# Kernel tuning notes

Hardware: AMD Instinct MI355X
Metric: run time of the kernel (lower is better)

The kernel has to match this reference:

```python
import jax, jax.numpy as jnp
import numpy as np

NUM_LAYERS = 4
HID = 512
BATCH = 32
SEQ = 2048


def log_g(x):
    # log of the g() activation used by minGRU: g(x) = x+0.5 for x>=0, sigmoid(x) for x<0
    return jnp.where(x >= 0, jnp.log(jax.nn.relu(x) + 0.5), -jax.nn.softplus(-x))


def parallel_scan_log(log_coeffs, log_values):
    # log_coeffs: (B, T, H), log_values: (B, T+1, H); returns h: (B, T, H)
    a_star = jnp.cumsum(jnp.pad(log_coeffs, ((0, 0), (1, 0), (0, 0))), axis=1)  # (B, T+1, H)
    log_h = a_star + jax.lax.cumlogsumexp(log_values - a_star, axis=1)
    return jnp.exp(log_h)[:, 1:]


def setup_inputs() -> dict:
    key = jax.random.key(0)
    ks = jax.random.split(key, 4)
    x = jax.random.normal(ks[0], (BATCH, SEQ, HID), dtype=jnp.float32)
    h0 = jax.random.uniform(ks[1], (NUM_LAYERS, BATCH, HID), dtype=jnp.float32)
    scale = 0.02
    Wz = jax.random.normal(ks[2], (NUM_LAYERS, HID, HID), dtype=jnp.float32) * scale
    Wh = jax.random.normal(ks[3], (NUM_LAYERS, HID, HID), dtype=jnp.float32) * scale
    bz = jnp.zeros((NUM_LAYERS, HID), dtype=jnp.float32)
    bh = jnp.zeros((NUM_LAYERS, HID), dtype=jnp.float32)
    gamma = jnp.ones((NUM_LAYERS, HID), dtype=jnp.float32)
    beta = jnp.zeros((NUM_LAYERS, HID), dtype=jnp.float32)
    return {"x": x, "h0": h0, "Wz": Wz, "bz": bz, "Wh": Wh, "bh": bh, "gamma": gamma, "beta": beta}


def layernorm(x, g, b, eps=1e-5):
    mu = jnp.mean(x, axis=-1, keepdims=True)
    var = jnp.mean((x - mu) ** 2, axis=-1, keepdims=True)
    return (x - mu) * jax.lax.rsqrt(var + eps) * g + b


def reference(x, h0, Wz, bz, Wh, bh, gamma, beta):
    cur = x
    hiddens = []
    L = Wz.shape[0]
    for i in range(L):
        k = jnp.einsum('btd,dh->bth', cur, Wz[i]) + bz[i]
        log_z = -jax.nn.softplus(-k)          # log(sigmoid(k)) = log(z)
        log_coeffs = -jax.nn.softplus(k)      # log(1-z)
        log_tilde_h = log_g(jnp.einsum('btd,dh->bth', cur, Wh[i]) + bh[i])
        log_h0 = log_g(h0[i])[:, None, :]     # (B, 1, H)
        log_values = jnp.concatenate([log_h0, log_z + log_tilde_h], axis=1)
        h = parallel_scan_log(log_coeffs, log_values)  # (B, T, H)
        hiddens.append(h[:, -1])
        out = layernorm(h, gamma[i], beta[i])
        cur = out + cur  # res_proj is Identity since input_size == hidden_size
    return cur, jnp.stack(hiddens, axis=0)
```

## Files before the change

kernel.cpp:

```cpp
#include <hip/hip_runtime.h>
#include <stdint.h>

typedef unsigned short u16;
typedef __bf16 bf16x8 __attribute__((ext_vector_type(8)));
typedef float f32x4 __attribute__((ext_vector_type(4)));

#define HID 512
#define BATCH 32
#define SEQ 2048
#define NLAYERS 4
#define BT (BATCH*SEQ)
#define CHUNKS 64
#define TC (SEQ/CHUNKS)

__device__ __forceinline__ float bf2f(uint32_t lo) {
  union { uint32_t u; float f; } c; c.u = lo << 16; return c.f;
}
__device__ __forceinline__ uint32_t f2bf(float f) {
  union { float f; uint32_t u; } c; c.f = f;
  return (c.u + 0x7fffu + ((c.u >> 16) & 1u)) >> 16;
}
__device__ __forceinline__ uint32_t pk_bf16(float lo, float hi) {
  uint32_t r;
  asm("v_cvt_pk_bf16_f32 %0, %1, %2" : "=v"(r) : "v"(lo), "v"(hi));
  return r;
}
__device__ __forceinline__ float fast_rcp(float x) { return __builtin_amdgcn_rcpf(x); }

__device__ __forceinline__ void gload_lds16(const u16* g, u16* l) {
  __builtin_amdgcn_global_load_lds((__attribute__((address_space(1))) void*)g,
                                   (__attribute__((address_space(3))) void*)l, 16, 0, 0);
}

__global__ __launch_bounds__(256) void conv_weights(const float* __restrict__ Wz,
                                                    const float* __restrict__ Wh,
                                                    u16* __restrict__ Wt) {
  __shared__ float tile[64][65];
  const int l = blockIdx.z;
  const int k0 = blockIdx.x * 64;
  const int n0 = blockIdx.y * 64;
  const float* W = (n0 < 512 ? Wz : Wh) + (size_t)l * HID * HID;
  const int nc0 = (n0 < 512) ? n0 : n0 - 512;
  const int tx = threadIdx.x & 63, ty = threadIdx.x >> 6;
  for (int r = ty; r < 64; r += 4) tile[r][tx] = W[(size_t)(k0 + r) * HID + nc0 + tx];
  __syncthreads();
  for (int r = ty; r < 64; r += 4)
    Wt[((size_t)l * 1024 + n0 + r) * HID + k0 + tx] = (u16)f2bf(tile[tx][r]);
}

__global__ __launch_bounds__(256) void conv_x(const float* __restrict__ x, u16* __restrict__ xb) {
  size_t i = ((size_t)blockIdx.x * 256 + threadIdx.x) * 4;
  float4 f = *(const float4*)(x + i);
  uint2 o;
  o.x = pk_bf16(f.x, f.y);
  o.y = pk_bf16(f.z, f.w);
  *(uint2*)(xb + i) = o;
}

__global__ __launch_bounds__(512) void gemm_av(const u16* __restrict__ Ab,
                                               const u16* __restrict__ Btw,
                                               const float* __restrict__ bz,
                                               const float* __restrict__ bhp,
                                               uint32_t* __restrict__ av,
                                               float* __restrict__ Ac,
                                               float* __restrict__ Bc) {
  __shared__ __align__(16) u16 As[2][2][8192];
  __shared__ __align__(16) u16 Bs[2][2][8192];

  const int bid = blockIdx.x;
  const int xcd = bid & 7, rr_ = bid >> 3;
  const int mt = (rr_ >> 2) * 8 + xcd;
  const int nt = rr_ & 3;
  const int m0 = mt * 256;

  const int tid = threadIdx.x;
  const int lane = tid & 63, wv = tid >> 6;
  const int wm = wv >> 2, wn = wv & 3;
  const int l15 = lane & 15, quad = lane >> 4;
  const int rx = l15 & 7;
  const int bhalf = wn >> 1;

  const int aro0 = l15 * 64 + ((quad ^ rx) * 8);
  const int aro1 = l15 * 64 + (((4 + quad) ^ rx) * 8);
  const int bro0 = ((wn & 1) * 64 + l15) * 64 + ((quad ^ rx) * 8);
  const int bro1 = ((wn & 1) * 64 + l15) * 64 + (((4 + quad) ^ rx) * 8);

  const int srow = tid >> 3;
  const int kslot = (lane & 7) ^ (srow & 7);
  const u16* aS = Ab + (size_t)(m0 + srow) * HID + kslot * 8;
  const int qb = (srow >> 5) & 1, jb = srow & 31;
  const u16* bS = Btw + (size_t)(qb * 512 + nt * 128 + jb) * HID + kslot * 8;

  f32x4 acc[8][4];
#pragma unroll
  for (int i = 0; i < 8; ++i)
#pragma unroll
    for (int j = 0; j < 4; ++j) acc[i][j] = (f32x4){0.f, 0.f, 0.f, 0.f};
  bf16x8 afr[4][2], bfr[4][2];

#define STG_A(T, H, D) if ((T) < 8) { \
    gload_lds16(aS + (size_t)((H)*65536 + (T)*64), &As[D][H][wv*512]); \
    gload_lds16(aS + (size_t)((H)*65536 + 32768 + (T)*64), &As[D][H][4096 + wv*512]); }
#define STG_B(T, H, D) if ((T) < 8) { \
    gload_lds16(bS + (size_t)((H)*32768 + (T)*64), &Bs[D][H][wv*512]); \
    gload_lds16(bS + (size_t)((H)*32768 + 16384 + (T)*64), &Bs[D][H][4096 + wv*512]); }
#define LDA4(D, MB) { \
    _Pragma("unroll") for (int m_ = 0; m_ < 4; ++m_) \
    _Pragma("unroll") for (int k_ = 0; k_ < 2; ++k_) \
      afr[m_][k_] = *(const bf16x8*)&As[D][wm][((MB)+m_)*1024 + (k_ ? aro1 : aro0)]; }
#define LDB2(D, NB) { \
    _Pragma("unroll") for (int n_ = 0; n_ < 2; ++n_) \
    _Pragma("unroll") for (int k_ = 0; k_ < 2; ++k_) \
      bfr[(NB)+n_][k_] = *(const bf16x8*)&Bs[D][bhalf][((NB)+n_)*1024 + (k_ ? bro1 : bro0)]; }
#define QUAD(MB, NB) { \
    _Pragma("unroll") for (int k_ = 0; k_ < 2; ++k_) \
    _Pragma("unroll") for (int m_ = 0; m_ < 4; ++m_) \
    _Pragma("unroll") for (int n_ = 0; n_ < 2; ++n_) \
      acc[(MB)+m_][(NB)+n_] = __builtin_amdgcn_mfma_f32_16x16x32_bf16( \
          afr[m_][k_], bfr[(NB)+n_][k_], acc[(MB)+m_][(NB)+n_], 0, 0, 0); }
#define PH_MID \
    __builtin_amdgcn_s_barrier(); \
    asm volatile("s_waitcnt lgkmcnt(0)" ::: "memory"); \
    __builtin_amdgcn_sched_barrier(0); \
    __builtin_amdgcn_s_setprio(1);
#define PH_END \
    __builtin_amdgcn_s_setprio(0); \
    __builtin_amdgcn_s_barrier(); \
    __builtin_amdgcn_sched_barrier(0);
#define PH_END_VM(N) \
    __builtin_amdgcn_s_setprio(0); \
    asm volatile("s_waitcnt vmcnt(" #N ")" ::: "memory"); \
    __builtin_amdgcn_s_barrier(); \
    __builtin_amdgcn_sched_barrier(0);

  STG_A(0, 0, 0); STG_A(0, 1, 0);
  STG_B(0, 0, 0); STG_B(0, 1, 0);
  STG_B(1, 0, 1); STG_B(1, 1, 1);
  asm volatile("s_waitcnt vmcnt(4)" ::: "memory");
  __builtin_amdgcn_s_barrier();
  __builtin_amdgcn_sched_barrier(0);

#pragma unroll
  for (int it = 0; it < 4; ++it) {
    const int ta = 2 * it, tb = 2 * it + 1;
    LDA4(0, 0); LDB2(0, 0); STG_A(tb, 0, 1);
    PH_MID; QUAD(0, 0); PH_END;
    LDB2(0, 2); STG_A(tb, 1, 1);
    PH_MID; QUAD(0, 2); PH_END;
    LDA4(0, 4); STG_B(ta + 2, 0, 0);
    PH_MID; QUAD(4, 0); PH_END;
    STG_B(ta + 2, 1, 0);
    PH_MID; QUAD(4, 2);
    if (it == 3) { PH_END_VM(0); } else { PH_END_VM(4); }
    LDA4(1, 0); LDB2(1, 0); STG_A(ta + 2, 0, 0);
    PH_MID; QUAD(0, 0); PH_END;
    LDB2(1, 2); STG_A(ta + 2, 1, 0);
    PH_MID; QUAD(0, 2); PH_END;
    LDA4(1, 4); STG_B(tb + 2, 0, 1);
    PH_MID; QUAD(4, 0); PH_END;
    STG_B(tb + 2, 1, 1);
    PH_MID; QUAD(4, 2); PH_END_VM(4);
  }

  const int colbase = nt * 128 + wn * 32;
  float bzv[2], bhv[2];
#pragma unroll
  for (int nf = 0; nf < 2; ++nf) {
    bzv[nf] = bz[colbase + nf * 16 + l15];
    bhv[nf] = bhp[colbase + nf * 16 + l15];
  }
  const int wrow0 = m0 + wm * 128;
  const int bb = wrow0 >> 11;
#pragma unroll
  for (int c = 0; c < 4; ++c) {
    const int cc = ((wrow0 + c * 32) & 2047) >> 5;
    const size_t abase = (size_t)(bb * CHUNKS + cc) * HID;
#pragma unroll
    for (int nf = 0; nf < 2; ++nf) {
      const int col = colbase + nf * 16 + l15;
      float aar[2][4], vvr[2][4], SA[2], SB[2];
#pragma unroll
      for (int hseg = 0; hseg < 2; ++hseg) {
        const int mf = 2 * c + hseg;
        float A = 1.f, Bv = 0.f;
#pragma unroll
        for (int r = 0; r < 4; ++r) {
          float kv = acc[mf][nf][r] + bzv[nf];
          float hv = acc[mf][nf + 2][r] + bhv[nf];
          float e = __expf(-kv);
          float inv = fast_rcp(1.f + e);
          float a = e * inv;
          float v = inv * ((hv >= 0.f) ? (hv + 0.5f) : fast_rcp(1.f + __expf(-hv)));
          aar[hseg][r] = a; vvr[hseg][r] = v;
          A *= a;
          Bv = a * Bv + v;
        }
        SA[hseg] = A; SB[hseg] = Bv;
      }
#pragma unroll
      for (int hseg = 0; hseg < 2; ++hseg) {
        float iA = SA[hseg], iB = SB[hseg];
        float pA = __shfl_up(iA, 16), pB = __shfl_up(iB, 16);
        if (quad >= 1) { iB = iA * pB + iB; iA = iA * pA; }
        pA = __shfl_up(iA, 32); pB = __shfl_up(iB, 32);
        if (quad >= 2) { iB = iA * pB + iB; iA = iA * pA; }
        SA[hseg] = iA; SB[hseg] = iB;
      }
      float E0A = __shfl_up(SA[0], 16), E0B = __shfl_up(SB[0], 16);
      if (quad == 0) { E0A = 1.f; E0B = 0.f; }
      float T0A = __shfl(SA[0], 48 + l15), T0B = __shfl(SB[0], 48 + l15);
      float e1A = __shfl_up(SA[1], 16), e1B = __shfl_up(SB[1], 16);
      if (quad == 0) { e1A = 1.f; e1B = 0.f; }
      float E1A = e1A * T0A, E1B = e1A * T0B + e1B;
#pragma unroll
      for (int hseg = 0; hseg < 2; ++hseg) {
        const float EA = hseg ? E1A : E0A;
        const float EB = hseg ? E1B : E0B;
        const int rbase = wrow0 + (2 * c + hseg) * 16 + quad * 4;
        float Ar = 1.f, Br = 0.f;
#pragma unroll
        for (int r = 0; r < 4; ++r) {
          Ar = aar[hseg][r] * Ar;
          Br = aar[hseg][r] * Br + vvr[hseg][r];
          float PA = Ar * EA;
          float PB = Ar * EB + Br;
          av[(size_t)(rbase + r) * HID + col] = pk_bf16(PA, PB);
          if (hseg == 1 && r == 3 && quad == 3) {
            Ac[abase + col] = PA;
            Bc[abase + col] = PB;
          }
        }
      }
    }
  }
#undef STG_A
#undef STG_B
#undef LDA4
#undef LDB2
#undef QUAD
#undef PH_MID
#undef PH_END
#undef PH_END_VM
}

__global__ __launch_bounds__(256) void scan_boundary(const float* __restrict__ Ac,
                                                     const float* __restrict__ Bc,
                                                     const float* __restrict__ h0,
                                                     float* __restrict__ hinit,
                                                     float* __restrict__ hid_out) {
  const int idx = blockIdx.x * 256 + threadIdx.x;
  const int b = idx >> 9, h = idx & 511;
  float x0 = h0[idx];
  float hr = (x0 >= 0.f) ? (x0 + 0.5f) : fast_rcp(1.f + __expf(-x0));
  for (int c = 0; c < CHUNKS; ++c) {
    size_t o = ((size_t)(b * CHUNKS + c)) * HID + h;
    hinit[o] = hr;
    hr = Ac[o] * hr + Bc[o];
  }
  hid_out[idx] = hr;
}

__global__ __launch_bounds__(512) void scan_apply(const uint32_t* av,
                                                  const float* __restrict__ hinit,
                                                  const u16* __restrict__ resb,
                                                  const float* __restrict__ gamma,
                                                  const float* __restrict__ beta,
                                                  u16* outb, float* outf) {
  const int b = blockIdx.y, c = blockIdx.x;
  const int lane = threadIdx.x & 63, wv = threadIdx.x >> 6;
  const size_t rowbase = (size_t)(b * SEQ + c * TC) * HID;
  const int h0c = lane * 8;

  const size_t hib = ((size_t)(b * CHUNKS + c)) * HID + h0c;
  const f32x4 hi0 = *(const f32x4*)&hinit[hib];
  const f32x4 hi1 = *(const f32x4*)&hinit[hib + 4];
  const f32x4 gm0 = *(const f32x4*)&gamma[h0c];
  const f32x4 gm1 = *(const f32x4*)&gamma[h0c + 4];
  const f32x4 be0 = *(const f32x4*)&beta[h0c];
  const f32x4 be1 = *(const f32x4*)&beta[h0c + 4];

#pragma unroll
  for (int i = 0; i < 4; ++i) {
    const int t = wv * 4 + i;
    const size_t o = rowbase + (size_t)t * HID + h0c;
    const uint4 p0 = *(const uint4*)(av + o);
    const uint4 p1 = *(const uint4*)(av + o + 4);
    const uint32_t pw[8] = {p0.x, p0.y, p0.z, p0.w, p1.x, p1.y, p1.z, p1.w};
    float hv[8];
#pragma unroll
    for (int j = 0; j < 8; ++j) {
      const float hij = (j < 4) ? hi0[j] : hi1[j - 4];
      hv[j] = bf2f(pw[j] & 0xffffu) * hij + bf2f(pw[j] >> 16);
    }
    float s = hv[0] + hv[1] + hv[2] + hv[3] + hv[4] + hv[5] + hv[6] + hv[7];
    float q = hv[0]*hv[0] + hv[1]*hv[1] + hv[2]*hv[2] + hv[3]*hv[3]
            + hv[4]*hv[4] + hv[5]*hv[5] + hv[6]*hv[6] + hv[7]*hv[7];
#pragma unroll
    for (int d = 32; d; d >>= 1) { s += __shfl_xor(s, d); q += __shfl_xor(q, d); }
    const float mu = s * (1.f / HID);
    const float rs = rsqrtf(q * (1.f / HID) - mu * mu + 1e-5f);
    const uint4 rr = *(const uint4*)(resb + o);
    const uint32_t rw[4] = {rr.x, rr.y, rr.z, rr.w};
    float y[8];
#pragma unroll
    for (int j = 0; j < 8; ++j) {
      const float gmv = (j < 4) ? gm0[j] : gm1[j - 4];
      const float bev = (j < 4) ? be0[j] : be1[j - 4];
      const float rv = bf2f((rw[j >> 1] >> ((j & 1) * 16)) & 0xffffu);
      y[j] = (hv[j] - mu) * rs * gmv + bev + rv;
    }
    if (outb) {
      uint4 ob;
      ob.x = pk_bf16(y[0], y[1]);
      ob.y = pk_bf16(y[2], y[3]);
      ob.z = pk_bf16(y[4], y[5]);
      ob.w = pk_bf16(y[6], y[7]);
      *(uint4*)(outb + o) = ob;
    }
    if (outf) {
      f32x4 o0 = {y[0], y[1], y[2], y[3]}, o1 = {y[4], y[5], y[6], y[7]};
      *(f32x4*)(outf + o) = o0;
      *(f32x4*)(outf + o + 4) = o1;
    }
  }
}

extern "C" void kernel_launch(void* const* d_in, const int* in_sizes, int n_in,
                              void* d_out, int out_size, void* d_ws, size_t ws_size,
                              hipStream_t stream) {
  (void)in_sizes; (void)n_in; (void)out_size; (void)ws_size;
  const float* x     = (const float*)d_in[0];
  const float* h0    = (const float*)d_in[1];
  const float* Wz    = (const float*)d_in[2];
  const float* bz    = (const float*)d_in[3];
  const float* Wh    = (const float*)d_in[4];
  const float* bh    = (const float*)d_in[5];
  const float* gamma = (const float*)d_in[6];
  const float* beta  = (const float*)d_in[7];

  float* outf = (float*)d_out;
  uint32_t* av = (uint32_t*)d_out;

  char* ws = (char*)d_ws;
  u16* curb = (u16*)ws;                                   size_t off = (size_t)BT * HID * 2;
  u16* Wt = (u16*)(ws + off);                             off += (size_t)NLAYERS * 1024 * HID * 2;
  float* Ac = (float*)(ws + off);                         off += (size_t)BATCH * CHUNKS * HID * 4;
  float* Bc = (float*)(ws + off);                         off += (size_t)BATCH * CHUNKS * HID * 4;
  float* hinit = (float*)(ws + off);

  hipLaunchKernelGGL(conv_weights, dim3(8, 16, NLAYERS), dim3(256), 0, stream, Wz, Wh, Wt);
  hipLaunchKernelGGL(conv_x, dim3(BT * HID / 1024), dim3(256), 0, stream, x, curb);

  for (int l = 0; l < NLAYERS; ++l) {
    const bool last = (l == NLAYERS - 1);
    hipLaunchKernelGGL(gemm_av, dim3(1024), dim3(512), 0, stream,
                       curb, Wt + (size_t)l * 1024 * HID, bz + l * HID, bh + l * HID,
                       av, Ac, Bc);
    hipLaunchKernelGGL(scan_boundary, dim3(BATCH * HID / 256), dim3(256), 0, stream,
                       Ac, Bc, h0 + (size_t)l * BATCH * HID, hinit,
                       outf + (size_t)BT * HID + (size_t)l * BATCH * HID);
    hipLaunchKernelGGL(scan_apply, dim3(CHUNKS, BATCH), dim3(512), 0, stream,
                       av, hinit, curb, gamma + l * HID, beta + l * HID,
                       last ? nullptr : curb, last ? outf : nullptr);
  }
}
```

Baseline: 835.5 us.

## Fuse chunk-boundary scan into scan_apply, recomputing prefix per block

Removes the separate scan_boundary kernel and its hinit buffer. Each scan_apply block now recomputes its own chunk-initial hidden state by serially combining the preceding chunks' (A,B) summaries, keeps it in LDS, and the last chunk also writes the final hidden output. This saves one launch per layer and a serialized low-parallelism kernel, at the cost of redundant O(c) prefix work per block, up to 63 dependent loads for late chunks.

```diff
diff --git a/kernel.cpp b/kernel.cpp
--- a/kernel.cpp
+++ b/kernel.cpp
@@ -243,37 +243,37 @@
 #undef PH_END_VM
 }
 
-__global__ __launch_bounds__(256) void scan_boundary(const float* __restrict__ Ac,
-                                                     const float* __restrict__ Bc,
-                                                     const float* __restrict__ h0,
-                                                     float* __restrict__ hinit,
-                                                     float* __restrict__ hid_out) {
-  const int idx = blockIdx.x * 256 + threadIdx.x;
-  const int b = idx >> 9, h = idx & 511;
-  float x0 = h0[idx];
-  float hr = (x0 >= 0.f) ? (x0 + 0.5f) : fast_rcp(1.f + __expf(-x0));
-  for (int c = 0; c < CHUNKS; ++c) {
-    size_t o = ((size_t)(b * CHUNKS + c)) * HID + h;
-    hinit[o] = hr;
-    hr = Ac[o] * hr + Bc[o];
-  }
-  hid_out[idx] = hr;
-}
-
 __global__ __launch_bounds__(512) void scan_apply(const uint32_t* av,
-                                                  const float* __restrict__ hinit,
+                                                  const float* __restrict__ Ac,
+                                                  const float* __restrict__ Bc,
+                                                  const float* __restrict__ h0p,
                                                   const u16* __restrict__ resb,
                                                   const float* __restrict__ gamma,
                                                   const float* __restrict__ beta,
-                                                  u16* outb, float* outf) {
+                                                  u16* outb, float* outf,
+                                                  float* __restrict__ hid_out) {
+  __shared__ float hinit_lds[HID];
   const int b = blockIdx.y, c = blockIdx.x;
   const int lane = threadIdx.x & 63, wv = threadIdx.x >> 6;
   const size_t rowbase = (size_t)(b * SEQ + c * TC) * HID;
   const int h0c = lane * 8;
 
-  const size_t hib = ((size_t)(b * CHUNKS + c)) * HID + h0c;
-  const f32x4 hi0 = *(const f32x4*)&hinit[hib];
-  const f32x4 hi1 = *(const f32x4*)&hinit[hib + 4];
+  {
+    const int h = threadIdx.x;
+    float x0 = h0p[(b << 9) + h];
+    float hr = (x0 >= 0.f) ? (x0 + 0.5f) : fast_rcp(1.f + __expf(-x0));
+    const size_t cb = (size_t)(b * CHUNKS) * HID + h;
+    for (int cp = 0; cp < c; ++cp)
+      hr = Ac[cb + (size_t)cp * HID] * hr + Bc[cb + (size_t)cp * HID];
+    hinit_lds[h] = hr;
+    if (c == CHUNKS - 1)
+      hid_out[(b << 9) + h] =
+          Ac[cb + (size_t)(CHUNKS - 1) * HID] * hr + Bc[cb + (size_t)(CHUNKS - 1) * HID];
+  }
+  __syncthreads();
+
+  const f32x4 hi0 = *(const f32x4*)&hinit_lds[h0c];
+  const f32x4 hi1 = *(const f32x4*)&hinit_lds[h0c + 4];
   const f32x4 gm0 = *(const f32x4*)&gamma[h0c];
   const f32x4 gm1 = *(const f32x4*)&gamma[h0c + 4];
   const f32x4 be0 = *(const f32x4*)&beta[h0c];
@@ -345,8 +345,7 @@
   u16* curb = (u16*)ws;                                   size_t off = (size_t)BT * HID * 2;
   u16* Wt = (u16*)(ws + off);                             off += (size_t)NLAYERS * 1024 * HID * 2;
   float* Ac = (float*)(ws + off);                         off += (size_t)BATCH * CHUNKS * HID * 4;
-  float* Bc = (float*)(ws + off);                         off += (size_t)BATCH * CHUNKS * HID * 4;
-  float* hinit = (float*)(ws + off);
+  float* Bc = (float*)(ws + off);
 
   hipLaunchKernelGGL(conv_weights, dim3(8, 16, NLAYERS), dim3(256), 0, stream, Wz, Wh, Wt);
   hipLaunchKernelGGL(conv_x, dim3(BT * HID / 1024), dim3(256), 0, stream, x, curb);
@@ -356,11 +355,10 @@
     hipLaunchKernelGGL(gemm_av, dim3(1024), dim3(512), 0, stream,
                        curb, Wt + (size_t)l * 1024 * HID, bz + l * HID, bh + l * HID,
                        av, Ac, Bc);
-    hipLaunchKernelGGL(scan_boundary, dim3(BATCH * HID / 256), dim3(256), 0, stream,
-                       Ac, Bc, h0 + (size_t)l * BATCH * HID, hinit,
+    hipLaunchKernelGGL(scan_apply, dim3(CHUNKS, BATCH), dim3(512), 0, stream,
+                       av, Ac, Bc, h0 + (size_t)l * BATCH * HID, curb,
+                       gamma + l * HID, beta + l * HID,
+                       last ? nullptr : curb, last ? outf : nullptr,
                        outf + (size_t)BT * HID + (size_t)l * BATCH * HID);
-    hipLaunchKernelGGL(scan_apply, dim3(CHUNKS, BATCH), dim3(512), 0, stream,
-                       av, hinit, curb, gamma + l * HID, beta + l * HID,
-                       last ? nullptr : curb, last ? outf : nullptr);
-  }
-}
+  }
+}
```

After: 890.1 us. 1.07x slower.
